# Performance work log

Hardware: AMD Instinct MI355X
Metric: run time of the kernel (lower is better)

Reference implementation:

```python
import jax, jax.numpy as jnp
import numpy as np

N = 100000
E = 1600000
F_IN = 32   # node_features
F_H = 32    # filters
F_OUT = 4


def setup_inputs() -> dict:
    key = jax.random.key(0)
    ks = jax.random.split(key, 24)
    inp = {
        'x': jax.random.normal(ks[0], (N, F_IN), dtype=jnp.float32),
        'edge_index': jax.random.randint(ks[1], (2, E), 0, N, dtype=jnp.int64),
        'edge_weight': jax.random.uniform(ks[2], (E,), dtype=jnp.float32),
        'H': jax.random.normal(ks[3], (N, F_H), dtype=jnp.float32),
    }
    # ChebConv params: W[k] for k in {0,1} (K=2), bias per conv.
    def cheb_params(kw, kb, fin):
        s = 1.0 / np.sqrt(fin)
        W = jax.random.uniform(kw, (2, fin, F_H), jnp.float32, -s, s)
        b = jax.random.uniform(kb, (F_H,), jnp.float32, -s, s)
        return W, b
    names = ['xz', 'hz', 'xr', 'hr', 'xh', 'hh']
    fins = [F_IN, F_H, F_IN, F_H, F_IN, F_H]
    for i, (nm, fin) in enumerate(zip(names, fins)):
        W, b = cheb_params(ks[4 + 2 * i], ks[5 + 2 * i], fin)
        inp['W' + nm] = W
        inp['b' + nm] = b
    s = 1.0 / np.sqrt(F_H)
    inp['lin_w'] = jax.random.uniform(ks[20], (F_H, F_OUT), jnp.float32, -s, s)
    inp['lin_b'] = jax.random.uniform(ks[21], (F_OUT,), jnp.float32, -s, s)
    return inp


def _cheb(x, src, dst, nw, W, b):
    # ChebConv, K=2, sym norm, lambda_max=2 => L_hat = -D^{-1/2} A D^{-1/2}
    # (diagonal of scaled Laplacian cancels exactly: 1 - 1 = 0).
    tx1 = -jax.ops.segment_sum(nw[:, None] * x[src], dst, num_segments=N)
    return x @ W[0] + tx1 @ W[1] + b


def reference(x, edge_index, edge_weight, H,
              Wxz, bxz, Whz, bhz, Wxr, bxr, Whr, bhr, Wxh, bxh, Whh, bhh,
              lin_w, lin_b):
    src, dst = edge_index[0], edge_index[1]
    # remove_self_loops equivalent: zero out self-loop weights
    w = jnp.where(src == dst, 0.0, edge_weight)
    deg = jax.ops.segment_sum(w, src, num_segments=N)
    dinv = jnp.where(deg > 0, jax.lax.rsqrt(jnp.maximum(deg, 1e-30)), 0.0)
    nw = dinv[src] * w * dinv[dst]  # per-edge sym-normalized weight

    Z = jax.nn.sigmoid(_cheb(x, src, dst, nw, Wxz, bxz) +
                       _cheb(H, src, dst, nw, Whz, bhz))
    R = jax.nn.sigmoid(_cheb(x, src, dst, nw, Wxr, bxr) +
                       _cheb(H, src, dst, nw, Whr, bhr))
    H_tilde = jnp.tanh(_cheb(x, src, dst, nw, Wxh, bxh) +
                       _cheb(H * R, src, dst, nw, Whh, bhh))
    h = Z * H + (1.0 - Z) * H_tilde
    out = jax.nn.relu(h) @ lin_w + lin_b
    return (out, h)
```

## Files before the change

### kernel.cpp

```cpp
#include <hip/hip_runtime.h>
#include <hip/hip_bf16.h>
#include <hip/hip_fp16.h>

typedef __hip_bfloat16 bf16;
typedef __attribute__((ext_vector_type(8))) short bf16x8;
typedef __attribute__((ext_vector_type(4))) float f32x4;

#define NN   100000
#define EE   1600000
#define FH   32
#define FOUT 4
#define NBD  782
#define NBS  196
#define CAPB 2432
#define CAPS 8960
#define CAP  64
#define BINBLK 256
#define BINTHR 1024
#define EPB  6250
#define MFMA16(a, b, c) __builtin_amdgcn_mfma_f32_16x16x32_bf16(a, b, c, 0, 0, 0)

__device__ __forceinline__ float b2f(bf16 v) { return __bfloat162float(v); }

__device__ __forceinline__ float ldf(const void* p, int i, int f32) {
    return f32 ? ((const float*)p)[i] : b2f(((const bf16*)p)[i]);
}
__device__ __forceinline__ int ldi(const void* p, int i, int i64f) {
    return i64f ? (int)(((const long long*)p)[i]) : ((const int*)p)[i];
}
__device__ __forceinline__ void stf(void* p, int i, int f32, float v) {
    if (f32) ((float*)p)[i] = v;
    else     ((bf16*)p)[i] = __float2bfloat16(v);
}
__device__ __forceinline__ float h2f(unsigned short u) {
    return __half2float(__ushort_as_half(u));
}
__device__ __forceinline__ unsigned short f2h16(float v) {
    return __half_as_ushort(__float2half(v));
}
__device__ __forceinline__ short f2bf(float v) {
    unsigned u = __float_as_uint(v);
    return (short)((u + 0x7FFFu + ((u >> 16) & 1u)) >> 16);
}
__device__ __forceinline__ unsigned q8(float v) {
    int q = (int)rintf(v * 16.f) + 128;
    q = q < 0 ? 0 : (q > 255 ? 255 : q);
    return (unsigned)q;
}
__device__ __forceinline__ float ub(unsigned w, int k) {
    return (float)((w >> (k * 8)) & 0xFFu);
}
__device__ __forceinline__ float4 bfly_g(float4 v) {
    v.x += __shfl_xor(v.x, 8);  v.y += __shfl_xor(v.y, 8);
    v.z += __shfl_xor(v.z, 8);  v.w += __shfl_xor(v.w, 8);
    v.x += __shfl_xor(v.x, 16); v.y += __shfl_xor(v.y, 16);
    v.z += __shfl_xor(v.z, 16); v.w += __shfl_xor(v.w, 16);
    return v;
}
__device__ __forceinline__ bf16x8 bfrag(const void* W, int f32, int cheb,
                                        int n, int kb) {
    bf16x8 r;
    #pragma unroll
    for (int j = 0; j < 8; j++)
        r[j] = f2bf(ldf(W, cheb * 1024 + (kb + j) * FH + n, f32));
    return r;
}

__global__ __launch_bounds__(256) void k_detect(const void* __restrict__ x,
                                                const void* __restrict__ ei,
                                                int* __restrict__ flg,
                                                int* __restrict__ binCur,
                                                int* __restrict__ binCurS) {
    __shared__ int s_f32[256], s_oddnz[256];
    int t = threadIdx.x;
    for (int i = t; i < NBD; i += 256) binCur[i] = i * CAPB;
    for (int i = t; i < NBS; i += 256) binCurS[i] = i * CAPS;
    float v = b2f(((const bf16*)x)[t]);
    s_f32[t] = (!isfinite(v)) || (fabsf(v) > 100.f);
    int w32 = ((const int*)ei)[t];
    s_oddnz[t] = ((t & 1) && (w32 != 0)) ? 1 : 0;
    __syncthreads();
    if (t == 0) {
        int f32 = 0, oddnz = 0;
        for (int i = 0; i < 256; i++) { f32 |= s_f32[i]; oddnz |= s_oddnz[i]; }
        flg[0] = f32;
        flg[1] = oddnz ? 0 : 1;
    }
}

__global__ __launch_bounds__(256) void k_pack(const void* __restrict__ x,
                                              const void* __restrict__ H,
                                              const int* __restrict__ flg,
                                              unsigned* __restrict__ xh,
                                              unsigned short* __restrict__ xh8) {
    int i = blockIdx.x * 256 + threadIdx.x;
    if (i >= NN * FH) return;
    int f32 = flg[0];
    float xv = ldf(x, i, f32);
    float hv = ldf(H, i, f32);
    xh[i] = ((unsigned)f2h16(hv) << 16) | f2h16(xv);
    xh8[i] = (unsigned short)((q8(hv) << 8) | q8(xv));
}

__global__ __launch_bounds__(BINTHR) void k_bin(const void* __restrict__ ei,
                                                const void* __restrict__ ew,
                                                const int* __restrict__ flg,
                                                int* __restrict__ binCur,
                                                int* __restrict__ binCurS,
                                                int2* __restrict__ dstRec,
                                                int* __restrict__ srcRec) {
    __shared__ int hD[NBD], bD[NBD], lofD[NBD];
    __shared__ int hS[NBS], bS[NBS], lofS[NBS];
    __shared__ int sc[BINTHR];
    __shared__ int2 stD[EPB];
    __shared__ int  stS[EPB];
    int t = threadIdx.x;
    for (int i = t; i < NBD; i += BINTHR) hD[i] = 0;
    for (int i = t; i < NBS; i += BINTHR) hS[i] = 0;
    __syncthreads();
    int e0 = blockIdx.x * EPB;
    int e1 = e0 + EPB; if (e1 > EE) e1 = EE;
    int f32 = flg[0], i64 = flg[1];
    for (int e = e0 + t; e < e1; e += BINTHR) {
        int s = ldi(ei, e, i64);
        int d = ldi(ei, EE + e, i64);
        atomicAdd(&hD[d >> 7], 1);
        atomicAdd(&hS[s >> 9], 1);
    }
    __syncthreads();
    for (int i = t; i < NBD; i += BINTHR)
        bD[i] = (hD[i] > 0) ? atomicAdd(&binCur[i], hD[i]) : 0;
    for (int i = t; i < NBS; i += BINTHR)
        bS[i] = (hS[i] > 0) ? atomicAdd(&binCurS[i], hS[i]) : 0;
    int vD = (t < NBD) ? hD[t] : 0;
    sc[t] = vD;
    __syncthreads();
    for (int ofs = 1; ofs < BINTHR; ofs <<= 1) {
        int u = (t >= ofs) ? sc[t - ofs] : 0;
        __syncthreads();
        sc[t] += u;
        __syncthreads();
    }
    if (t < NBD) { lofD[t] = sc[t] - vD; hD[t] = 0; }
    __syncthreads();
    int vS = (t < NBS) ? hS[t] : 0;
    sc[t] = vS;
    __syncthreads();
    for (int ofs = 1; ofs < BINTHR; ofs <<= 1) {
        int u = (t >= ofs) ? sc[t - ofs] : 0;
        __syncthreads();
        sc[t] += u;
        __syncthreads();
    }
    if (t < NBS) { lofS[t] = sc[t] - vS; hS[t] = 0; }
    __syncthreads();
    for (int e = e0 + t; e < e1; e += BINTHR) {
        int s = ldi(ei, e, i64);
        int d = ldi(ei, EE + e, i64);
        float w = (s == d) ? 0.f : ldf(ew, e, f32);
        int wh = (int)(f2h16(w) & 0x7FFFu);
        int bd = d >> 7, bs = s >> 9;
        int rd = atomicAdd(&hD[bd], 1);
        int rs = atomicAdd(&hS[bs], 1);
        stD[lofD[bd] + rd] = make_int2((int)(((unsigned)s << 15) | wh),
                                       (bd << 8) | (d & 127));
        stS[lofS[bs] + rs] = (int)(((unsigned)bs << 24) |
                                   ((unsigned)(s & 511) << 15) | (unsigned)wh);
    }
    __syncthreads();
    int tot = e1 - e0;
    for (int i = t; i < tot; i += BINTHR) {
        int2 r = stD[i];
        int bin = ((unsigned)r.y) >> 8;
        int g = bD[bin] + (i - lofD[bin]);
        if (g < (bin + 1) * CAPB) dstRec[g] = make_int2(r.x, r.y & 127);
        int u = stS[i];
        int sbin = ((unsigned)u) >> 24;
        int gs = bS[sbin] + (i - lofS[sbin]);
        if (gs < (sbin + 1) * CAPS) srcRec[gs] = u & 0xFFFFFF;
    }
}

__global__ __launch_bounds__(256) void k_fillb(const int* __restrict__ binCur,
                                               const int2* __restrict__ dstRec,
                                               int* __restrict__ cursor,
                                               int* __restrict__ ell) {
    __shared__ int lCur[128];
    __shared__ int lEll[128 * CAP];
    int b = blockIdx.x, t = threadIdx.x;
    if (t < 128) lCur[t] = 0;
    __syncthreads();
    int cnt = binCur[b] - b * CAPB;
    if (cnt > CAPB) cnt = CAPB;
    for (int i = t; i < cnt; i += 256) {
        int2 r = dstRec[b * CAPB + i];
        int slot = atomicAdd(&lCur[r.y], 1);
        if (slot < CAP) lEll[r.y * CAP + slot] = r.x;
    }
    __syncthreads();
    int nodeBase = b * 128;
    for (int i = t; i < 128 * CAP; i += 256) {
        int node = nodeBase + (i >> 6);
        if (node < NN && (i & 63) < lCur[i >> 6])
            ell[(size_t)node * CAP + (i & (CAP - 1))] = lEll[i];
    }
    if (t < 128 && nodeBase + t < NN) {
        int c = lCur[t]; if (c > CAP) c = CAP;
        cursor[nodeBase + t] = c;
    }
}

__global__ __launch_bounds__(256) void k_degb(const int* __restrict__ binCurS,
                                              const int* __restrict__ srcRec,
                                              float* __restrict__ dinv) {
    __shared__ float lDeg[512];
    int b = blockIdx.x, t = threadIdx.x;
    lDeg[t] = 0.f; lDeg[t + 256] = 0.f;
    __syncthreads();
    int cnt = binCurS[b] - b * CAPS;
    if (cnt > CAPS) cnt = CAPS;
    for (int i = t; i < cnt; i += 256) {
        int r = srcRec[b * CAPS + i];
        atomicAdd(&lDeg[(r >> 15) & 511], h2f((unsigned short)(r & 0x7FFF)));
    }
    __syncthreads();
    #pragma unroll
    for (int k = 0; k < 2; k++) {
        int li = t + k * 256;
        int node = b * 512 + li;
        if (node < NN) {
            float dv = lDeg[li];
            dinv[node] = (dv > 0.f) ? rsqrtf(dv) : 0.f;
        }
    }
}

__global__ __launch_bounds__(256) void k_gather1(const int* __restrict__ cursor,
                                                 const int* __restrict__ ell,
                                                 const float* __restrict__ dinv,
                                                 const unsigned short* __restrict__ xh8,
                                                 unsigned* __restrict__ axah) {
    int t = threadIdx.x;
    int node = blockIdx.x * 8 + (t >> 5);
    if (node >= NN) return;
    int f = t & 31;
    int g = f >> 3, c = f & 7;
    int cnt = cursor[node];
    size_t base = (size_t)node * CAP;
    float4 ax = {0.f, 0.f, 0.f, 0.f}, ah = {0.f, 0.f, 0.f, 0.f};
    float cs = 0.f;
    for (int j = 0; j < cnt; j += 4) {
        int jj = j + g;
        float coef = 0.f; int s = 0;
        if (jj < cnt) {
            int wrd = ell[base + jj];
            s = ((unsigned)wrd) >> 15;
            coef = dinv[s] * h2f((unsigned short)(wrd & 0x7FFF));
        }
        cs += coef;
        uint2 pv = ((const uint2*)xh8)[s * 8 + c];
        ax.x += coef * ub(pv.x, 0);
        ah.x += coef * ub(pv.x, 1);
        ax.y += coef * ub(pv.x, 2);
        ah.y += coef * ub(pv.x, 3);
        ax.z += coef * ub(pv.y, 0);
        ah.z += coef * ub(pv.y, 1);
        ax.w += coef * ub(pv.y, 2);
        ah.w += coef * ub(pv.y, 3);
    }
    ax = bfly_g(ax); ah = bfly_g(ah);
    cs += __shfl_xor(cs, 8);
    cs += __shfl_xor(cs, 16);
    if (g == 0) {
        float dd = -dinv[node];
        float bias = 8.f * cs;
        uint4 o;
        o.x = ((unsigned)f2h16(dd * (ah.x * 0.0625f - bias)) << 16)
            | f2h16(dd * (ax.x * 0.0625f - bias));
        o.y = ((unsigned)f2h16(dd * (ah.y * 0.0625f - bias)) << 16)
            | f2h16(dd * (ax.y * 0.0625f - bias));
        o.z = ((unsigned)f2h16(dd * (ah.z * 0.0625f - bias)) << 16)
            | f2h16(dd * (ax.z * 0.0625f - bias));
        o.w = ((unsigned)f2h16(dd * (ah.w * 0.0625f - bias)) << 16)
            | f2h16(dd * (ax.w * 0.0625f - bias));
        ((uint4*)(axah + (size_t)node * FH))[c] = o;
    }
}

__global__ __launch_bounds__(256) void k_zr_mfma(
    const unsigned* __restrict__ xh, const unsigned* __restrict__ axah,
    const int* __restrict__ flg,
    const void* __restrict__ Wxz, const void* __restrict__ bxz,
    const void* __restrict__ Whz, const void* __restrict__ bhz,
    const void* __restrict__ Wxr, const void* __restrict__ bxr,
    const void* __restrict__ Whr, const void* __restrict__ bhr,
    float* __restrict__ Z, unsigned short* __restrict__ hr16) {
    int t = threadIdx.x;
    int lane = t & 63, wv = t >> 6;
    int f32 = flg[0];
    int c = lane & 15, quad = lane >> 4, kb = quad * 8;
    int nodeBase = blockIdx.x * 64 + wv * 16;
    int nm = nodeBase + c; if (nm >= NN) nm = NN - 1;

    bf16x8 fx, fHH, fAX, fAH;
    {
        const uint4* p = (const uint4*)(xh + (size_t)nm * FH + kb);
        uint4 a = p[0], b = p[1];
        unsigned wd[8] = {a.x, a.y, a.z, a.w, b.x, b.y, b.z, b.w};
        #pragma unroll
        for (int j = 0; j < 8; j++) {
            fx[j]  = f2bf(h2f((unsigned short)(wd[j] & 0xFFFF)));
            fHH[j] = f2bf(h2f((unsigned short)(wd[j] >> 16)));
        }
    }
    {
        const uint4* p = (const uint4*)(axah + (size_t)nm * FH + kb);
        uint4 a = p[0], b = p[1];
        unsigned wd[8] = {a.x, a.y, a.z, a.w, b.x, b.y, b.z, b.w};
        #pragma unroll
        for (int j = 0; j < 8; j++) {
            fAX[j] = f2bf(h2f((unsigned short)(wd[j] & 0xFFFF)));
            fAH[j] = f2bf(h2f((unsigned short)(wd[j] >> 16)));
        }
    }

    float bz0 = ldf(bxz, c, f32) + ldf(bhz, c, f32);
    float bz1 = ldf(bxz, c + 16, f32) + ldf(bhz, c + 16, f32);
    float br0 = ldf(bxr, c, f32) + ldf(bhr, c, f32);
    float br1 = ldf(bxr, c + 16, f32) + ldf(bhr, c + 16, f32);
    f32x4 az0 = {bz0, bz0, bz0, bz0}, az1 = {bz1, bz1, bz1, bz1};
    f32x4 ar0 = {br0, br0, br0, br0}, ar1 = {br1, br1, br1, br1};

    az0 = MFMA16(fx,  bfrag(Wxz, f32, 0, c, kb),      az0);
    az0 = MFMA16(fAX, bfrag(Wxz, f32, 1, c, kb),      az0);
    az0 = MFMA16(fHH, bfrag(Whz, f32, 0, c, kb),      az0);
    az0 = MFMA16(fAH, bfrag(Whz, f32, 1, c, kb),      az0);
    az1 = MFMA16(fx,  bfrag(Wxz, f32, 0, c + 16, kb), az1);
    az1 = MFMA16(fAX, bfrag(Wxz, f32, 1, c + 16, kb), az1);
    az1 = MFMA16(fHH, bfrag(Whz, f32, 0, c + 16, kb), az1);
    az1 = MFMA16(fAH, bfrag(Whz, f32, 1, c + 16, kb), az1);
    ar0 = MFMA16(fx,  bfrag(Wxr, f32, 0, c, kb),      ar0);
    ar0 = MFMA16(fAX, bfrag(Wxr, f32, 1, c, kb),      ar0);
    ar0 = MFMA16(fHH, bfrag(Whr, f32, 0, c, kb),      ar0);
    ar0 = MFMA16(fAH, bfrag(Whr, f32, 1, c, kb),      ar0);
    ar1 = MFMA16(fx,  bfrag(Wxr, f32, 0, c + 16, kb), ar1);
    ar1 = MFMA16(fAX, bfrag(Wxr, f32, 1, c + 16, kb), ar1);
    ar1 = MFMA16(fHH, bfrag(Whr, f32, 0, c + 16, kb), ar1);
    ar1 = MFMA16(fAH, bfrag(Whr, f32, 1, c + 16, kb), ar1);

    #pragma unroll
    for (int tl = 0; tl < 2; tl++) {
        f32x4 az = tl ? az1 : az0, ar = tl ? ar1 : ar0;
        int f = c + 16 * tl;
        #pragma unroll
        for (int r = 0; r < 4; r++) {
            int node = nodeBase + quad * 4 + r;
            if (node < NN) {
                float zv = 1.f / (1.f + expf(-az[r]));
                float rv = 1.f / (1.f + expf(-ar[r]));
                float Hv = h2f((unsigned short)(xh[(size_t)node * FH + f] >> 16));
                Z[(size_t)node * FH + f] = zv;
                hr16[(size_t)node * FH + f] = f2h16(Hv * rv);
            }
        }
    }
}

__global__ __launch_bounds__(256) void k_gather2(const int* __restrict__ cursor,
                                                 const int* __restrict__ ell,
                                                 const float* __restrict__ dinv,
                                                 const unsigned short* __restrict__ hr16,
                                                 unsigned short* __restrict__ ahr16) {
    int t = threadIdx.x;
    int node = blockIdx.x * 8 + (t >> 5);
    if (node >= NN) return;
    int f = t & 31;
    int g = f >> 3, c = f & 7;
    int cnt = cursor[node];
    size_t base = (size_t)node * CAP;
    float4 acc = {0.f, 0.f, 0.f, 0.f};
    for (int j = 0; j < cnt; j += 4) {
        int jj = j + g;
        float coef = 0.f; int s = 0;
        if (jj < cnt) {
            int wrd = ell[base + jj];
            s = ((unsigned)wrd) >> 15;
            coef = dinv[s] * h2f((unsigned short)(wrd & 0x7FFF));
        }
        ushort4 hv = ((const ushort4*)hr16)[s * 8 + c];
        acc.x += coef * h2f(hv.x);
        acc.y += coef * h2f(hv.y);
        acc.z += coef * h2f(hv.z);
        acc.w += coef * h2f(hv.w);
    }
    acc = bfly_g(acc);
    if (g == 0) {
        float dd = -dinv[node];
        ushort4 o = {f2h16(dd * acc.x), f2h16(dd * acc.y),
                     f2h16(dd * acc.z), f2h16(dd * acc.w)};
        ((ushort4*)(ahr16 + (size_t)node * FH))[c] = o;
    }
}

__global__ __launch_bounds__(256) void k_final_mfma(
    const unsigned* __restrict__ xh, const unsigned* __restrict__ axah,
    const int* __restrict__ flg,
    const float* __restrict__ Z, const unsigned short* __restrict__ hr16,
    const unsigned short* __restrict__ ahr16,
    const void* __restrict__ Wxh, const void* __restrict__ bxh,
    const void* __restrict__ Whh, const void* __restrict__ bhh,
    const void* __restrict__ lin_w, const void* __restrict__ lin_b,
    void* __restrict__ out) {
    __shared__ float srh[64][FH];
    __shared__ float slw[FH * FOUT];
    __shared__ float slb[FOUT];

    int t = threadIdx.x;
    int lane = t & 63, wv = t >> 6;
    int f32 = flg[0];
    int c = lane & 15, quad = lane >> 4, kb = quad * 8;
    int nodeBase = blockIdx.x * 64 + wv * 16;
    int nm = nodeBase + c; if (nm >= NN) nm = NN - 1;

    if (t < FH * FOUT) slw[t] = ldf(lin_w, t, f32);
    if (t < FOUT) slb[t] = ldf(lin_b, t, f32);

    bf16x8 fx, fAX, fHR, fAHR;
    {
        const uint4* p = (const uint4*)(xh + (size_t)nm * FH + kb);
        uint4 a = p[0], b = p[1];
        unsigned wd[8] = {a.x, a.y, a.z, a.w, b.x, b.y, b.z, b.w};
        #pragma unroll
        for (int j = 0; j < 8; j++)
            fx[j] = f2bf(h2f((unsigned short)(wd[j] & 0xFFFF)));
    }
    {
        const uint4* p = (const uint4*)(axah + (size_t)nm * FH + kb);
        uint4 a = p[0], b = p[1];
        unsigned wd[8] = {a.x, a.y, a.z, a.w, b.x, b.y, b.z, b.w};
        #pragma unroll
        for (int j = 0; j < 8; j++)
            fAX[j] = f2bf(h2f((unsigned short)(wd[j] & 0xFFFF)));
    }
    {
        const uint4* p = (const uint4*)(hr16 + (size_t)nm * FH + kb);
        uint4 a = p[0];
        unsigned wd[4] = {a.x, a.y, a.z, a.w};
        #pragma unroll
        for (int j = 0; j < 8; j++)
            fHR[j] = f2bf(h2f((unsigned short)((wd[j >> 1] >> ((j & 1) * 16)) & 0xFFFF)));
    }
    {
        const uint4* p = (const uint4*)(ahr16 + (size_t)nm * FH + kb);
        uint4 a = p[0];
        unsigned wd[4] = {a.x, a.y, a.z, a.w};
        #pragma unroll
        for (int j = 0; j < 8; j++)
            fAHR[j] = f2bf(h2f((unsigned short)((wd[j >> 1] >> ((j & 1) * 16)) & 0xFFFF)));
    }

    float bh0 = ldf(bxh, c, f32) + ldf(bhh, c, f32);
    float bh1 = ldf(bxh, c + 16, f32) + ldf(bhh, c + 16, f32);
    f32x4 a0 = {bh0, bh0, bh0, bh0}, a1 = {bh1, bh1, bh1, bh1};

    a0 = MFMA16(fx,   bfrag(Wxh, f32, 0, c, kb),      a0);
    a0 = MFMA16(fAX,  bfrag(Wxh, f32, 1, c, kb),      a0);
    a0 = MFMA16(fHR,  bfrag(Whh, f32, 0, c, kb),      a0);
    a0 = MFMA16(fAHR, bfrag(Whh, f32, 1, c, kb),      a0);
    a1 = MFMA16(fx,   bfrag(Wxh, f32, 0, c + 16, kb), a1);
    a1 = MFMA16(fAX,  bfrag(Wxh, f32, 1, c + 16, kb), a1);
    a1 = MFMA16(fHR,  bfrag(Whh, f32, 0, c + 16, kb), a1);
    a1 = MFMA16(fAHR, bfrag(Whh, f32, 1, c + 16, kb), a1);

    #pragma unroll
    for (int tl = 0; tl < 2; tl++) {
        f32x4 a = tl ? a1 : a0;
        int f = c + 16 * tl;
        #pragma unroll
        for (int r = 0; r < 4; r++) {
            int node = nodeBase + quad * 4 + r;
            if (node < NN) {
                float ht = tanhf(a[r]);
                float zv = Z[(size_t)node * FH + f];
                float Hv = h2f((unsigned short)(xh[(size_t)node * FH + f] >> 16));
                float hval = zv * Hv + (1.f - zv) * ht;
                stf(out, NN * FOUT + node * FH + f, f32, hval);
                srh[wv * 16 + quad * 4 + r][f] = hval > 0.f ? hval : 0.f;
            }
        }
    }
    __syncthreads();

    int nl = t >> 2, fo = t & 3;
    int node2 = blockIdx.x * 64 + nl;
    if (node2 < NN) {
        float acc = slb[fo];
        #pragma unroll
        for (int k = 0; k < FH; k++) acc += srh[nl][k] * slw[k * FOUT + fo];
        stf(out, node2 * FOUT + fo, f32, acc);
    }
}

extern "C" void kernel_launch(void* const* d_in, const int* in_sizes, int n_in,
                              void* d_out, int out_size, void* d_ws, size_t ws_size,
                              hipStream_t stream) {
    const void* x   = d_in[0];
    const void* ei  = d_in[1];
    const void* ew  = d_in[2];
    const void* H   = d_in[3];
    const void* Wxz = d_in[4];
    const void* bxz = d_in[5];
    const void* Whz = d_in[6];
    const void* bhz = d_in[7];
    const void* Wxr = d_in[8];
    const void* bxr = d_in[9];
    const void* Whr = d_in[10];
    const void* bhr = d_in[11];
    const void* Wxh = d_in[12];
    const void* bxh = d_in[13];
    const void* Whh = d_in[14];
    const void* bhh = d_in[15];
    const void* lnw = d_in[16];
    const void* lnb = d_in[17];

    char* base = (char*)d_ws;
    int*            flg     = (int*)base;            base += 64;
    int*            binCur  = (int*)base;            base += (NBD * 4 + 63) & ~63;
    int*            binCurS = (int*)base;            base += (NBS * 4 + 63) & ~63;
    float*          dinv    = (float*)base;          base += (size_t)NN * 4;
    int*            cursor  = (int*)base;            base += (size_t)NN * 4;
    unsigned*       xh      = (unsigned*)base;       base += (size_t)NN * FH * 4;
    unsigned short* xh8     = (unsigned short*)base; base += (size_t)NN * FH * 2;
    char*           aliasRg = base;
    unsigned*       axah    = (unsigned*)base;       base += (size_t)NN * FH * 4;
    float*          Z       = (float*)base;          base += (size_t)NN * FH * 4;
    unsigned short* hr16    = (unsigned short*)base; base += (size_t)NN * FH * 2;
    unsigned short* ahr16   = (unsigned short*)base; base += (size_t)NN * FH * 2;
    int*            ell     = (int*)base;
    int2*           dstRec  = (int2*)aliasRg;
    int*            srcRec  = (int*)(aliasRg + (size_t)NBD * CAPB * 8);

    const int pb   = (NN * FH + 255) / 256;
    const int n8b  = (NN + 7) / 8;
    const int n64b = (NN + 63) / 64;

    k_detect<<<1, 256, 0, stream>>>(x, ei, flg, binCur, binCurS);
    k_pack<<<pb, 256, 0, stream>>>(x, H, flg, xh, xh8);
    k_bin<<<BINBLK, BINTHR, 0, stream>>>(ei, ew, flg, binCur, binCurS,
                                         dstRec, srcRec);
    k_fillb<<<NBD, 256, 0, stream>>>(binCur, dstRec, cursor, ell);
    k_degb<<<NBS, 256, 0, stream>>>(binCurS, srcRec, dinv);
    k_gather1<<<n8b, 256, 0, stream>>>(cursor, ell, dinv, xh8, axah);
    k_zr_mfma<<<n64b, 256, 0, stream>>>(xh, axah, flg, Wxz, bxz, Whz, bhz,
                                        Wxr, bxr, Whr, bhr, Z, hr16);
    k_gather2<<<n8b, 256, 0, stream>>>(cursor, ell, dinv, hr16, ahr16);
    k_final_mfma<<<n64b, 256, 0, stream>>>(xh, axah, flg, Z, hr16, ahr16,
                                           Wxh, bxh, Whh, bhh, lnw, lnb, d_out);
}
```

Baseline: 302.1 us.

## Pre-transpose weights to bf16 once and unroll gather loop by two edges

Adds a small kernel that converts all six ChebConv weight tensors to bf16 in transposed layout, so each MFMA B-fragment becomes a single 16-byte vector load instead of eight strided scalar loads with per-element conversion. Separately, the first gather kernel now handles two edges per lane per iteration, putting two independent index and feature loads in flight to hide latency. This costs an extra launch, a small workspace buffer, and more registers in the gather loop.

```diff
diff --git a/kernel.cpp b/kernel.cpp
--- a/kernel.cpp
+++ b/kernel.cpp
@@ -57,13 +57,8 @@
     v.z += __shfl_xor(v.z, 16); v.w += __shfl_xor(v.w, 16);
     return v;
 }
-__device__ __forceinline__ bf16x8 bfrag(const void* W, int f32, int cheb,
-                                        int n, int kb) {
-    bf16x8 r;
-    #pragma unroll
-    for (int j = 0; j < 8; j++)
-        r[j] = f2bf(ldf(W, cheb * 1024 + (kb + j) * FH + n, f32));
-    return r;
+__device__ __forceinline__ bf16x8 bfragT(const short* __restrict__ wt, int idx) {
+    return *(const bf16x8*)(wt + idx);
 }
 
 __global__ __launch_bounds__(256) void k_detect(const void* __restrict__ x,
@@ -86,6 +81,21 @@
         flg[0] = f32;
         flg[1] = oddnz ? 0 : 1;
     }
+}
+
+__global__ __launch_bounds__(256) void k_prepw(
+    const void* __restrict__ W0, const void* __restrict__ W1,
+    const void* __restrict__ W2, const void* __restrict__ W3,
+    const void* __restrict__ W4, const void* __restrict__ W5,
+    const int* __restrict__ flg, short* __restrict__ wt) {
+    int i = blockIdx.x * 256 + threadIdx.x;
+    if (i >= 6 * 2048) return;
+    int mat = i >> 11;
+    int r = i & 2047;
+    int cheb = r >> 10, k = (r >> 5) & 31, n = r & 31;
+    const void* W = (mat == 0) ? W0 : (mat == 1) ? W1 : (mat == 2) ? W2
+                  : (mat == 3) ? W3 : (mat == 4) ? W4 : W5;
+    wt[(((mat << 1) + cheb) << 10) + n * 32 + k] = f2bf(ldf(W, r, flg[0]));
 }
 
 __global__ __launch_bounds__(256) void k_pack(const void* __restrict__ x,
@@ -249,24 +259,25 @@
     size_t base = (size_t)node * CAP;
     float4 ax = {0.f, 0.f, 0.f, 0.f}, ah = {0.f, 0.f, 0.f, 0.f};
     float cs = 0.f;
-    for (int j = 0; j < cnt; j += 4) {
-        int jj = j + g;
-        float coef = 0.f; int s = 0;
-        if (jj < cnt) {
-            int wrd = ell[base + jj];
-            s = ((unsigned)wrd) >> 15;
-            coef = dinv[s] * h2f((unsigned short)(wrd & 0x7FFF));
-        }
-        cs += coef;
-        uint2 pv = ((const uint2*)xh8)[s * 8 + c];
-        ax.x += coef * ub(pv.x, 0);
-        ah.x += coef * ub(pv.x, 1);
-        ax.y += coef * ub(pv.x, 2);
-        ah.y += coef * ub(pv.x, 3);
-        ax.z += coef * ub(pv.y, 0);
-        ah.z += coef * ub(pv.y, 1);
-        ax.w += coef * ub(pv.y, 2);
-        ah.w += coef * ub(pv.y, 3);
+    for (int j = 0; j < cnt; j += 8) {
+        int jj0 = j + g, jj1 = j + 4 + g;
+        int wrd0 = (jj0 < cnt) ? ell[base + jj0] : 0;
+        int wrd1 = (jj1 < cnt) ? ell[base + jj1] : 0;
+        int s0 = ((unsigned)wrd0) >> 15;
+        int s1 = ((unsigned)wrd1) >> 15;
+        float c0 = dinv[s0] * h2f((unsigned short)(wrd0 & 0x7FFF));
+        float c1 = dinv[s1] * h2f((unsigned short)(wrd1 & 0x7FFF));
+        uint2 p0 = ((const uint2*)xh8)[s0 * 8 + c];
+        uint2 p1 = ((const uint2*)xh8)[s1 * 8 + c];
+        cs += c0 + c1;
+        ax.x += c0 * ub(p0.x, 0) + c1 * ub(p1.x, 0);
+        ah.x += c0 * ub(p0.x, 1) + c1 * ub(p1.x, 1);
+        ax.y += c0 * ub(p0.x, 2) + c1 * ub(p1.x, 2);
+        ah.y += c0 * ub(p0.x, 3) + c1 * ub(p1.x, 3);
+        ax.z += c0 * ub(p0.y, 0) + c1 * ub(p1.y, 0);
+        ah.z += c0 * ub(p0.y, 1) + c1 * ub(p1.y, 1);
+        ax.w += c0 * ub(p0.y, 2) + c1 * ub(p1.y, 2);
+        ah.w += c0 * ub(p0.y, 3) + c1 * ub(p1.y, 3);
     }
     ax = bfly_g(ax); ah = bfly_g(ah);
     cs += __shfl_xor(cs, 8);
@@ -289,11 +300,9 @@
 
 __global__ __launch_bounds__(256) void k_zr_mfma(
     const unsigned* __restrict__ xh, const unsigned* __restrict__ axah,
-    const int* __restrict__ flg,
-    const void* __restrict__ Wxz, const void* __restrict__ bxz,
-    const void* __restrict__ Whz, const void* __restrict__ bhz,
-    const void* __restrict__ Wxr, const void* __restrict__ bxr,
-    const void* __restrict__ Whr, const void* __restrict__ bhr,
+    const int* __restrict__ flg, const short* __restrict__ wt,
+    const void* __restrict__ bxz, const void* __restrict__ bhz,
+    const void* __restrict__ bxr, const void* __restrict__ bhr,
     float* __restrict__ Z, unsigned short* __restrict__ hr16) {
     int t = threadIdx.x;
     int lane = t & 63, wv = t >> 6;
@@ -331,22 +340,24 @@
     f32x4 az0 = {bz0, bz0, bz0, bz0}, az1 = {bz1, bz1, bz1, bz1};
     f32x4 ar0 = {br0, br0, br0, br0}, ar1 = {br1, br1, br1, br1};
 
-    az0 = MFMA16(fx,  bfrag(Wxz, f32, 0, c, kb),      az0);
-    az0 = MFMA16(fAX, bfrag(Wxz, f32, 1, c, kb),      az0);
-    az0 = MFMA16(fHH, bfrag(Whz, f32, 0, c, kb),      az0);
-    az0 = MFMA16(fAH, bfrag(Whz, f32, 1, c, kb),      az0);
-    az1 = MFMA16(fx,  bfrag(Wxz, f32, 0, c + 16, kb), az1);
-    az1 = MFMA16(fAX, bfrag(Wxz, f32, 1, c + 16, kb), az1);
-    az1 = MFMA16(fHH, bfrag(Whz, f32, 0, c + 16, kb), az1);
-    az1 = MFMA16(fAH, bfrag(Whz, f32, 1, c + 16, kb), az1);
-    ar0 = MFMA16(fx,  bfrag(Wxr, f32, 0, c, kb),      ar0);
-    ar0 = MFMA16(fAX, bfrag(Wxr, f32, 1, c, kb),      ar0);
-    ar0 = MFMA16(fHH, bfrag(Whr, f32, 0, c, kb),      ar0);
-    ar0 = MFMA16(fAH, bfrag(Whr, f32, 1, c, kb),      ar0);
-    ar1 = MFMA16(fx,  bfrag(Wxr, f32, 0, c + 16, kb), ar1);
-    ar1 = MFMA16(fAX, bfrag(Wxr, f32, 1, c + 16, kb), ar1);
-    ar1 = MFMA16(fHH, bfrag(Whr, f32, 0, c + 16, kb), ar1);
-    ar1 = MFMA16(fAH, bfrag(Whr, f32, 1, c + 16, kb), ar1);
+    int i0 = c * 32 + kb;
+    int i1 = (c + 16) * 32 + kb;
+    az0 = MFMA16(fx,  bfragT(wt, 0 * 1024 + i0), az0);
+    az0 = MFMA16(fAX, bfragT(wt, 1 * 1024 + i0), az0);
+    az0 = MFMA16(fHH, bfragT(wt, 2 * 1024 + i0), az0);
+    az0 = MFMA16(fAH, bfragT(wt, 3 * 1024 + i0), az0);
+    az1 = MFMA16(fx,  bfragT(wt, 0 * 1024 + i1), az1);
+    az1 = MFMA16(fAX, bfragT(wt, 1 * 1024 + i1), az1);
+    az1 = MFMA16(fHH, bfragT(wt, 2 * 1024 + i1), az1);
+    az1 = MFMA16(fAH, bfragT(wt, 3 * 1024 + i1), az1);
+    ar0 = MFMA16(fx,  bfragT(wt, 4 * 1024 + i0), ar0);
+    ar0 = MFMA16(fAX, bfragT(wt, 5 * 1024 + i0), ar0);
+    ar0 = MFMA16(fHH, bfragT(wt, 6 * 1024 + i0), ar0);
+    ar0 = MFMA16(fAH, bfragT(wt, 7 * 1024 + i0), ar0);
+    ar1 = MFMA16(fx,  bfragT(wt, 4 * 1024 + i1), ar1);
+    ar1 = MFMA16(fAX, bfragT(wt, 5 * 1024 + i1), ar1);
+    ar1 = MFMA16(fHH, bfragT(wt, 6 * 1024 + i1), ar1);
+    ar1 = MFMA16(fAH, bfragT(wt, 7 * 1024 + i1), ar1);
 
     #pragma unroll
     for (int tl = 0; tl < 2; tl++) {
@@ -404,11 +415,10 @@
 
 __global__ __launch_bounds__(256) void k_final_mfma(
     const unsigned* __restrict__ xh, const unsigned* __restrict__ axah,
-    const int* __restrict__ flg,
+    const int* __restrict__ flg, const short* __restrict__ wt,
     const float* __restrict__ Z, const unsigned short* __restrict__ hr16,
     const unsigned short* __restrict__ ahr16,
-    const void* __restrict__ Wxh, const void* __restrict__ bxh,
-    const void* __restrict__ Whh, const void* __restrict__ bhh,
+    const void* __restrict__ bxh, const void* __restrict__ bhh,
     const void* __restrict__ lin_w, const void* __restrict__ lin_b,
     void* __restrict__ out) {
     __shared__ float srh[64][FH];
@@ -463,14 +473,16 @@
     float bh1 = ldf(bxh, c + 16, f32) + ldf(bhh, c + 16, f32);
     f32x4 a0 = {bh0, bh0, bh0, bh0}, a1 = {bh1, bh1, bh1, bh1};
 
-    a0 = MFMA16(fx,   bfrag(Wxh, f32, 0, c, kb),      a0);
-    a0 = MFMA16(fAX,  bfrag(Wxh, f32, 1, c, kb),      a0);
-    a0 = MFMA16(fHR,  bfrag(Whh, f32, 0, c, kb),      a0);
-    a0 = MFMA16(fAHR, bfrag(Whh, f32, 1, c, kb),      a0);
-    a1 = MFMA16(fx,   bfrag(Wxh, f32, 0, c + 16, kb), a1);
-    a1 = MFMA16(fAX,  bfrag(Wxh, f32, 1, c + 16, kb), a1);
-    a1 = MFMA16(fHR,  bfrag(Whh, f32, 0, c + 16, kb), a1);
-    a1 = MFMA16(fAHR, bfrag(Whh, f32, 1, c + 16, kb), a1);
+    int i0 = c * 32 + kb;
+    int i1 = (c + 16) * 32 + kb;
+    a0 = MFMA16(fx,   bfragT(wt,  8 * 1024 + i0), a0);
+    a0 = MFMA16(fAX,  bfragT(wt,  9 * 1024 + i0), a0);
+    a0 = MFMA16(fHR,  bfragT(wt, 10 * 1024 + i0), a0);
+    a0 = MFMA16(fAHR, bfragT(wt, 11 * 1024 + i0), a0);
+    a1 = MFMA16(fx,   bfragT(wt,  8 * 1024 + i1), a1);
+    a1 = MFMA16(fAX,  bfragT(wt,  9 * 1024 + i1), a1);
+    a1 = MFMA16(fHR,  bfragT(wt, 10 * 1024 + i1), a1);
+    a1 = MFMA16(fAHR, bfragT(wt, 11 * 1024 + i1), a1);
 
     #pragma unroll
     for (int tl = 0; tl < 2; tl++) {
@@ -529,6 +541,7 @@
     int*            binCurS = (int*)base;            base += (NBS * 4 + 63) & ~63;
     float*          dinv    = (float*)base;          base += (size_t)NN * 4;
     int*            cursor  = (int*)base;            base += (size_t)NN * 4;
+    short*          wt      = (short*)base;          base += (12288 * 2 + 63) & ~63;
     unsigned*       xh      = (unsigned*)base;       base += (size_t)NN * FH * 4;
     unsigned short* xh8     = (unsigned short*)base; base += (size_t)NN * FH * 2;
     char*           aliasRg = base;
@@ -545,15 +558,16 @@
     const int n64b = (NN + 63) / 64;
 
     k_detect<<<1, 256, 0, stream>>>(x, ei, flg, binCur, binCurS);
+    k_prepw<<<48, 256, 0, stream>>>(Wxz, Whz, Wxr, Whr, Wxh, Whh, flg, wt);
     k_pack<<<pb, 256, 0, stream>>>(x, H, flg, xh, xh8);
     k_bin<<<BINBLK, BINTHR, 0, stream>>>(ei, ew, flg, binCur, binCurS,
                                          dstRec, srcRec);
     k_fillb<<<NBD, 256, 0, stream>>>(binCur, dstRec, cursor, ell);
     k_degb<<<NBS, 256, 0, stream>>>(binCurS, srcRec, dinv);
     k_gather1<<<n8b, 256, 0, stream>>>(cursor, ell, dinv, xh8, axah);
-    k_zr_mfma<<<n64b, 256, 0, stream>>>(xh, axah, flg, Wxz, bxz, Whz, bhz,
-                                        Wxr, bxr, Whr, bhr, Z, hr16);
+    k_zr_mfma<<<n64b, 256, 0, stream>>>(xh, axah, flg, wt,
+                                        bxz, bhz, bxr, bhr, Z, hr16);
     k_gather2<<<n8b, 256, 0, stream>>>(cursor, ell, dinv, hr16, ahr16);
-    k_final_mfma<<<n64b, 256, 0, stream>>>(xh, axah, flg, Z, hr16, ahr16,
-                                           Wxh, bxh, Whh, bhh, lnw, lnb, d_out);
-}
+    k_final_mfma<<<n64b, 256, 0, stream>>>(xh, axah, flg, wt, Z, hr16, ahr16,
+                                           bxh, bhh, lnw, lnb, d_out);
+}
```

After: 281.6 us. 6.8% less time.
